# Optimization experiments

Hardware: AMD Instinct MI355X
Metric: run time of the kernel (lower is better)

Reference implementation:

```python
import jax, jax.numpy as jnp
import numpy as np

DIM = 256
HEADS = 8
DIM_HEAD = 32
INNER = HEADS * DIM_HEAD  # 256
SCALE = DIM_HEAD ** -0.5
NEG = -100.0

MASK0 = jnp.array([[0., 0., 0., NEG],
                   [0., 0., NEG, 0.],
                   [0., NEG, 0., 0.],
                   [NEG, 0., 0., 0.]], dtype=jnp.float32)
MASK1 = jnp.array([[0., NEG, 0., NEG],
                   [NEG, 0., NEG, 0.],
                   [NEG, NEG, NEG, NEG],
                   [NEG, NEG, NEG, NEG]], dtype=jnp.float32)


def setup_inputs() -> dict:
    key = jax.random.key(0)
    ks = jax.random.split(key, 8)
    b, p, d = 8, 3136, DIM
    return {
        "x": jax.random.normal(ks[0], (b, p, d), jnp.float32),
        "y": jax.random.normal(ks[1], (b, p, d), jnp.float32),
        "Wqkv_z": jax.random.normal(ks[2], (3 * INNER, d), jnp.float32) * 0.02,
        "Wout_z": jax.random.normal(ks[3], (d, INNER), jnp.float32) * 0.02,
        "bout_z": jnp.zeros((d,), jnp.float32),
        "Wqkv_z1": jax.random.normal(ks[4], (3 * INNER, d), jnp.float32) * 0.02,
        "Wout_z1": jax.random.normal(ks[5], (d, INNER), jnp.float32) * 0.02,
        "bout_z1": jnp.zeros((d,), jnp.float32),
    }


def _attn_stage(z, Wqkv, Wout, bout, mask):
    # z: [b, p, n=4, d]
    b, p, n, d = z.shape
    qkv = jnp.einsum('bpnd,ed->bpne', z, Wqkv)  # [b,p,4,3*inner]
    q, k, v = jnp.split(qkv, 3, axis=-1)
    def heads(t):  # [b,p,n,inner] -> [b,p,h,n,dh]
        return t.reshape(b, p, n, HEADS, DIM_HEAD).transpose(0, 1, 3, 2, 4)
    q, k, v = heads(q), heads(k), heads(v)
    dots = jnp.einsum('bphid,bphjd->bphij', q, k) * SCALE + mask
    attn = jax.nn.softmax(dots, axis=-1)
    out = jnp.einsum('bphij,bphjd->bphid', attn, v)
    out = out.transpose(0, 1, 3, 2, 4).reshape(b, p, n, INNER)
    return jnp.einsum('bpne,de->bpnd', out, Wout) + bout


def reference(x, y, Wqkv_z, Wout_z, bout_z, Wqkv_z1, Wout_z1, bout_z1):
    b, p, d = x.shape
    rgb_g = jnp.mean(x, axis=1, keepdims=True)    # avg_pool1d over p == mean
    dep_g = jnp.mean(y, axis=1, keepdims=True)
    rgb_g = jnp.broadcast_to(rgb_g, (b, p, d))
    dep_g = jnp.broadcast_to(dep_g, (b, p, d))
    z = jnp.stack([x, y, rgb_g, dep_g], axis=2)   # [b,p,4,d]
    z_out = _attn_stage(z, Wqkv_z, Wout_z, bout_z, MASK0)
    z_out1 = _attn_stage(z_out, Wqkv_z1, Wout_z1, bout_z1, MASK1)
    x1 = z_out1[:, :, 0, :]
    y1 = z_out1[:, :, 1, :]
    return (x1, y1)
```

## Files before the change

### kernel.cpp

```cpp
#include <hip/hip_runtime.h>
#include <hip/hip_fp8.h>

typedef unsigned short u16;
typedef unsigned int   u32;
typedef unsigned char  u8;
typedef short bf16x8 __attribute__((ext_vector_type(8)));
typedef float f32x16 __attribute__((ext_vector_type(16)));

#define NB    8
#define NP    3136
#define DIM   256
#define PTILE 16
#define NEGM  (-100.0f)
#define QKSCALE 0.17677669529663687f

#define LDS_SZ  65536
#define Q0B     16384
#define K0B     32768
#define P0B     49152
#define A1LB    32768
#define Q1B     49152
#define P1B     32768
#define AO1LB   16384

__device__ __forceinline__ float bflo(u32 w) { return __uint_as_float(w << 16); }
__device__ __forceinline__ float bfhi(u32 w) { return __uint_as_float(w & 0xffff0000u); }

__device__ __forceinline__ u32 cvt_pk(float a, float b) {
  u32 r;
  asm("v_cvt_pk_bf16_f32 %0, %1, %2" : "=v"(r) : "v"(a), "v"(b));
  return r;
}
__device__ __forceinline__ u8 f2fp8(float v) {
  __hip_fp8_e4m3 t(v);
  return *(u8*)&t;
}
__device__ __forceinline__ float fp82f(u8 bv) {
  __hip_fp8_e4m3 t;
  *(u8*)&t = bv;
  return (float)t;
}
__device__ __forceinline__ bf16x8 expand8(uint2 u) {
  const float s = 0.00390625f;
  float f0 = fp82f((u8)(u.x))       * s, f1 = fp82f((u8)(u.x >> 8))  * s;
  float f2 = fp82f((u8)(u.x >> 16)) * s, f3 = fp82f((u8)(u.x >> 24)) * s;
  float f4 = fp82f((u8)(u.y))       * s, f5 = fp82f((u8)(u.y >> 8))  * s;
  float f6 = fp82f((u8)(u.y >> 16)) * s, f7 = fp82f((u8)(u.y >> 24)) * s;
  union { bf16x8 v; uint4 w; } r;
  r.w.x = cvt_pk(f0, f1); r.w.y = cvt_pk(f2, f3);
  r.w.z = cvt_pk(f4, f5); r.w.w = cvt_pk(f6, f7);
  return r.v;
}

__device__ __forceinline__ void phase_fence() { __builtin_amdgcn_sched_barrier(0); }

template<int MASKI>
__device__ __forceinline__ float maskv(int i, int j) {
  if (MASKI == 0) return ((i ^ j) == 3) ? NEGM : 0.f;
  return (i >= 2 || ((i ^ j) & 1)) ? NEGM : 0.f;
}

#define FRAG(nt, ks) ((((size_t)(nt) * 16 + (ks)) * 64 + lane) * 8)

__device__ __forceinline__ void pack4(const float* __restrict__ W,
                                      u16* __restrict__ hi, u16* __restrict__ lo,
                                      int is_qkv, int pair0, int tid) {
  const int p    = pair0 + (tid >> 6);
  const int lane = tid & 63;
  const int nt = p >> 4, ks = p & 15;
  const int n  = nt * 32 + (lane & 31);
  const int k0 = ks * 16 + ((lane >> 5) << 3);
  const float scale = (is_qkv && n < 256) ? QKSCALE : 1.0f;
  const float* src = W + (size_t)n * 256 + k0;
  const size_t o = (((size_t)nt * 16 + ks) * 64 + lane) * 8;
#pragma unroll
  for (int j = 0; j < 8; j++) {
    float v = src[j] * scale;
    u32 wh = cvt_pk(v, v);
    hi[o + j] = (u16)wh;
    if (lo) lo[o + j] = (u16)cvt_pk(v - bflo(wh), 0.f);
  }
}

__global__ __launch_bounds__(256)
void prep1(const float* __restrict__ x, const float* __restrict__ y,
           float* __restrict__ part,
           const float* __restrict__ wqkv0, u16* __restrict__ wq0_hi,
           const float* __restrict__ wout1, u16* __restrict__ wo1_hi, u16* __restrict__ wo1_lo,
           const float* __restrict__ wqkv1, const float* __restrict__ wout0,
           float* __restrict__ Wc,
           const float* __restrict__ bout0, float* __restrict__ bq) {
  __shared__ float srow[256];
  const int bid = blockIdx.x;
  const int tid = threadIdx.x;
  if (bid < 512) {
    const int chunk = bid & 31;
    const int ab = bid >> 5;
    const int b = ab & 7;
    const float* src = (ab >> 3) ? y : x;
    float s = 0.f;
    const int p0 = chunk * 98;
    for (int i = 0; i < 98; i++)
      s += src[((size_t)b * NP + p0 + i) * DIM + tid];
    part[((size_t)ab * 32 + chunk) * DIM + tid] = s;
  } else if (bid < 608) {
    pack4(wqkv0, wq0_hi, nullptr, 1, (bid - 512) * 4, tid);
  } else if (bid < 640) {
    pack4(wout1, wo1_hi, wo1_lo, 0, (bid - 608) * 4, tid);
  } else if (bid < 1408) {
    const int n = bid - 640;
    srow[tid] = wqkv1[(size_t)n * 256 + tid];
    __syncthreads();
    float acc = 0.f;
#pragma unroll 8
    for (int d = 0; d < 256; d++)
      acc += srow[d] * wout0[(size_t)d * 256 + tid];
    Wc[(size_t)n * 256 + tid] = acc;
  } else {
    const int n = (bid - 1408) * 256 + tid;
    float s = 0.f;
    for (int d = 0; d < 256; d += 4) {
      const float4 w = *(const float4*)(wqkv1 + (size_t)n * 256 + d);
      const float4 bv = *(const float4*)(bout0 + d);
      s += w.x * bv.x + w.y * bv.y + w.z * bv.z + w.w * bv.w;
    }
    bq[n] = (n < 256) ? s * QKSCALE : s;
  }
}

__global__ __launch_bounds__(256)
void prep2(const float* __restrict__ part, float* __restrict__ g,
           const float* __restrict__ Wc, u16* __restrict__ wc_hi, u16* __restrict__ wc_lo) {
  const int bid = blockIdx.x;
  const int tid = threadIdx.x;
  if (bid < 16) {
    float s = 0.f;
    for (int c = 0; c < 32; c++) s += part[((size_t)bid * 32 + c) * DIM + tid];
    g[bid * DIM + tid] = s * (1.0f / 3136.0f);
  } else {
    pack4(Wc, wc_hi, wc_lo, 1, (bid - 16) * 4, tid);
  }
}

__global__ __launch_bounds__(256)
void prep3(const float* __restrict__ g, const float* __restrict__ wqkv0,
           float* __restrict__ qkvg) {
  __shared__ float srow[256];
  const int bt = blockIdx.x;
  const int b = bt >> 1, t = bt & 1;
  const int tid = threadIdx.x;
  srow[tid] = g[(t == 0 ? b : 8 + b) * 256 + tid];
  __syncthreads();
#pragma unroll
  for (int s = 0; s < 3; s++) {
    const int e = s * 256 + tid;
    float acc = 0.f;
    for (int d = 0; d < 256; d += 4) {
      const float4 w = *(const float4*)(wqkv0 + (size_t)e * 256 + d);
      acc += w.x * srow[d] + w.y * srow[d + 1] + w.z * srow[d + 2] + w.w * srow[d + 3];
    }
    qkvg[(size_t)bt * 768 + e] = (e < 256) ? acc * QKSCALE : acc;
  }
}

__global__ __launch_bounds__(512, 4)
void fused_kernel(const float* __restrict__ x, const float* __restrict__ y,
                  const float* __restrict__ qkvg, float* __restrict__ outp,
                  const u16* __restrict__ wq0_hi,
                  const u16* __restrict__ wc_hi,  const u16* __restrict__ wc_lo,
                  const u16* __restrict__ wo1_hi, const u16* __restrict__ wo1_lo,
                  const float* __restrict__ bq,   const float* __restrict__ bout1) {
  extern __shared__ char lds[];
  const int tid  = threadIdx.x;
  const int lane = tid & 63;
  const int wave = tid >> 6;
  const int cl   = lane & 31;
  const int rh5  = lane >> 5;
  const int kgrp = rh5 << 3;
  const int b    = blockIdx.y;
  const int pos0 = blockIdx.x * PTILE;
  const int apos = wave * 2 + rh5;
  const int ah   = (lane >> 2) & 7;
  const int adq  = lane & 3;
  const float* qg = qkvg + (size_t)(b * 2) * 768;

  {
    const int r   = tid >> 4;
    const int cb  = (tid & 15) * 16;
    const int pos = pos0 + (r >> 1);
    const float* src = ((r & 1) ? y : x) + ((size_t)b * NP + pos) * DIM;
#pragma unroll
    for (int u = 0; u < 4; u++) {
      const int col = cb + u * 4;
      float4 v = *(const float4*)(src + col);
      uint2 hw;
      hw.x = cvt_pk(v.x, v.y);
      hw.y = cvt_pk(v.z, v.w);
      *(uint2*)(lds + ((r * 512 + col * 2) ^ ((r & 15) << 4))) = hw;
    }
  }
  __syncthreads();
  phase_fence();

  f32x16 av;
  {
    f32x16 aq, ak;
#pragma unroll
    for (int i = 0; i < 16; i++) { aq[i] = 0.f; ak[i] = 0.f; av[i] = 0.f; }
#pragma unroll 2
    for (int ks = 0; ks < 16; ks++) {
      const int k0 = ks * 16 + kgrp;
      bf16x8 ahf = *(const bf16x8*)(lds + ((cl * 512 + k0 * 2) ^ ((cl & 15) << 4)));
      bf16x8 bQ = *(const bf16x8*)(wq0_hi + FRAG(wave, ks));
      bf16x8 bK = *(const bf16x8*)(wq0_hi + FRAG(8 + wave, ks));
      bf16x8 bV = *(const bf16x8*)(wq0_hi + FRAG(16 + wave, ks));
      __builtin_amdgcn_s_setprio(1);
      aq = __builtin_amdgcn_mfma_f32_32x32x16_bf16(ahf, bQ, aq, 0, 0, 0);
      ak = __builtin_amdgcn_mfma_f32_32x32x16_bf16(ahf, bK, ak, 0, 0, 0);
      av = __builtin_amdgcn_mfma_f32_32x32x16_bf16(ahf, bV, av, 0, 0, 0);
      __builtin_amdgcn_s_setprio(0);
    }
    const int sw0 = ((cl ^ wave) & 7) << 3;
    const int bQd = Q0B + wave * 2048 + cl * 64;
    const int bKd = K0B + wave * 2048 + cl * 64;
#pragma unroll
    for (int gq = 0; gq < 4; gq++) {
      const int p20 = 8 * gq + 4 * rh5;
      uint2 wv;
      wv.x = cvt_pk(aq[4 * gq + 0], aq[4 * gq + 1]);
      wv.y = cvt_pk(aq[4 * gq + 2], aq[4 * gq + 3]);
      *(uint2*)(lds + bQd + ((p20 * 2) ^ sw0)) = wv;
      wv.x = cvt_pk(ak[4 * gq + 0], ak[4 * gq + 1]);
      wv.y = cvt_pk(ak[4 * gq + 2], ak[4 * gq + 3]);
      *(uint2*)(lds + bKd + ((p20 * 2) ^ sw0)) = wv;
    }
  }
  __syncthreads();
  phase_fence();

  {
    const int e0 = ah * 32 + adq * 8;
    float dots[4][4];
#pragma unroll
    for (int i = 0; i < 4; i++)
#pragma unroll
      for (int j = 0; j < 4; j++) dots[i][j] = 0.f;
#pragma unroll 2
    for (int dd = 0; dd < 8; dd++) {
      const int d = adq * 8 + dd;
      const int sw = ((d ^ ah) & 7) << 3;
      u32 qw = *(const u32*)(lds + Q0B + ah * 2048 + d * 64 + ((apos * 4) ^ sw));
      u32 kw = *(const u32*)(lds + K0B + ah * 2048 + d * 64 + ((apos * 4) ^ sw));
      float q[4] = { bflo(qw), bfhi(qw), qg[e0 + dd], qg[768 + e0 + dd] };
      float k[4] = { bflo(kw), bfhi(kw), qg[256 + e0 + dd], qg[1024 + e0 + dd] };
#pragma unroll
      for (int i = 0; i < 4; i++)
#pragma unroll
        for (int j = 0; j < 4; j++) dots[i][j] += q[i] * k[j];
    }
#pragma unroll
    for (int i = 0; i < 4; i++)
#pragma unroll
      for (int j = 0; j < 4; j++) {
        float s = dots[i][j];
        s += __shfl_xor(s, 1);
        s += __shfl_xor(s, 2);
        dots[i][j] = s + maskv<0>(i, j);
      }
    if (adq == 0) {
#pragma unroll
      for (int i = 0; i < 4; i++) {
        const float mx = fmaxf(fmaxf(dots[i][0], dots[i][1]), fmaxf(dots[i][2], dots[i][3]));
        const float e0_ = __expf(dots[i][0] - mx), e1_ = __expf(dots[i][1] - mx);
        const float e2_ = __expf(dots[i][2] - mx), e3_ = __expf(dots[i][3] - mx);
        const float inv = 1.f / (e0_ + e1_ + e2_ + e3_);
        float4 pv_ = { e0_ * inv, e1_ * inv, e2_ * inv, e3_ * inv };
        *(float4*)(lds + P0B + ((apos * 8 + ah) * 4 + i) * 16) = pv_;
      }
    }
  }
  __syncthreads();
  phase_fence();

  {
    const float vg2 = qg[512 + wave * 32 + cl];
    const float vg3 = qg[768 + 512 + wave * 32 + cl];
    const int c = wave * 32 + cl;
#pragma unroll
    for (int gq = 0; gq < 4; gq++) {
#pragma unroll
      for (int pp = 0; pp < 2; pp++) {
        const int pos = 4 * gq + 2 * rh5 + pp;
        const float v0 = av[4 * gq + 2 * pp], v1 = av[4 * gq + 2 * pp + 1];
#pragma unroll
        for (int i = 0; i < 4; i++) {
          float4 pi = *(const float4*)(lds + P0B + ((pos * 8 + wave) * 4 + i) * 16);
          const float o = pi.x * v0 + pi.y * v1 + pi.z * vg2 + pi.w * vg3;
          const int R = pos * 4 + i;
          const u32 hw_ = cvt_pk(o, o);
          *(u16*)(lds + ((R * 512 + c * 2) ^ ((R & 15) << 4))) = (u16)hw_;
          *(u8*)(lds + A1LB + ((R * 256 + c) ^ ((R & 15) << 3))) =
              f2fp8((o - bflo(hw_)) * 256.f);
        }
      }
    }
  }
  __syncthreads();
  phase_fence();

  {
    f32x16 aq0, aq1;
#pragma unroll
    for (int i = 0; i < 16; i++) { aq0[i] = 0.f; aq1[i] = 0.f; }
#pragma unroll 1
    for (int ks = 0; ks < 16; ks++) {
      const int k0 = ks * 16 + kgrp;
      bf16x8 ah0 = *(const bf16x8*)(lds + ((cl * 512 + k0 * 2) ^ ((cl & 15) << 4)));
      bf16x8 ah1 = *(const bf16x8*)(lds + (((32 + cl) * 512 + k0 * 2) ^ (((32 + cl) & 15) << 4)));
      bf16x8 bh = *(const bf16x8*)(wc_hi + FRAG(wave, ks));
      bf16x8 bl = *(const bf16x8*)(wc_lo + FRAG(wave, ks));
      __builtin_amdgcn_s_setprio(1);
      aq0 = __builtin_amdgcn_mfma_f32_32x32x16_bf16(ah0, bh, aq0, 0, 0, 0);
      aq0 = __builtin_amdgcn_mfma_f32_32x32x16_bf16(ah0, bl, aq0, 0, 0, 0);
      aq1 = __builtin_amdgcn_mfma_f32_32x32x16_bf16(ah1, bh, aq1, 0, 0, 0);
      aq1 = __builtin_amdgcn_mfma_f32_32x32x16_bf16(ah1, bl, aq1, 0, 0, 0);
      __builtin_amdgcn_s_setprio(0);
    }
    const float qb = bq[wave * 32 + cl];
    const int swq = ((cl ^ wave) & 7) << 3;
    const int bQ1 = Q1B + wave * 2048 + cl * 64;
#pragma unroll
    for (int gq = 0; gq < 4; gq++) {
      const int posA = 2 * gq + rh5;
      *(u32*)(lds + bQ1 + ((posA * 4) ^ swq)) =
          cvt_pk(aq0[4 * gq] + qb, aq0[4 * gq + 1] + qb);
      *(u32*)(lds + bQ1 + (((posA + 8) * 4) ^ swq)) =
          cvt_pk(aq1[4 * gq] + qb, aq1[4 * gq + 1] + qb);
    }
  }
  phase_fence();
  uint2 kp0[4], kp1[4];
  {
    f32x16 ak0, ak1;
#pragma unroll
    for (int i = 0; i < 16; i++) { ak0[i] = 0.f; ak1[i] = 0.f; }
#pragma unroll 1
    for (int ks = 0; ks < 16; ks++) {
      const int k0 = ks * 16 + kgrp;
      bf16x8 ah0 = *(const bf16x8*)(lds + ((cl * 512 + k0 * 2) ^ ((cl & 15) << 4)));
      bf16x8 ah1 = *(const bf16x8*)(lds + (((32 + cl) * 512 + k0 * 2) ^ (((32 + cl) & 15) << 4)));
      bf16x8 bh = *(const bf16x8*)(wc_hi + FRAG(8 + wave, ks));
      bf16x8 bl = *(const bf16x8*)(wc_lo + FRAG(8 + wave, ks));
      __builtin_amdgcn_s_setprio(1);
      ak0 = __builtin_amdgcn_mfma_f32_32x32x16_bf16(ah0, bh, ak0, 0, 0, 0);
      ak0 = __builtin_amdgcn_mfma_f32_32x32x16_bf16(ah0, bl, ak0, 0, 0, 0);
      ak1 = __builtin_amdgcn_mfma_f32_32x32x16_bf16(ah1, bh, ak1, 0, 0, 0);
      ak1 = __builtin_amdgcn_mfma_f32_32x32x16_bf16(ah1, bl, ak1, 0, 0, 0);
      __builtin_amdgcn_s_setprio(0);
    }
    const float kb = bq[256 + wave * 32 + cl];
#pragma unroll
    for (int gq = 0; gq < 4; gq++) {
      kp0[gq].x = cvt_pk(ak0[4 * gq + 0] + kb, ak0[4 * gq + 1] + kb);
      kp0[gq].y = cvt_pk(ak0[4 * gq + 2] + kb, ak0[4 * gq + 3] + kb);
      kp1[gq].x = cvt_pk(ak1[4 * gq + 0] + kb, ak1[4 * gq + 1] + kb);
      kp1[gq].y = cvt_pk(ak1[4 * gq + 2] + kb, ak1[4 * gq + 3] + kb);
    }
  }
  phase_fence();
  f32x16 av0, av1;
  {
#pragma unroll
    for (int i = 0; i < 16; i++) { av0[i] = 0.f; av1[i] = 0.f; }
#pragma unroll 1
    for (int ks = 0; ks < 16; ks++) {
      const int k0 = ks * 16 + kgrp;
      bf16x8 ah0 = *(const bf16x8*)(lds + ((cl * 512 + k0 * 2) ^ ((cl & 15) << 4)));
      bf16x8 ah1 = *(const bf16x8*)(lds + (((32 + cl) * 512 + k0 * 2) ^ (((32 + cl) & 15) << 4)));
      uint2 u0 = *(const uint2*)(lds + A1LB + ((cl * 256 + k0) ^ ((cl & 15) << 3)));
      uint2 u1 = *(const uint2*)(lds + A1LB + (((32 + cl) * 256 + k0) ^ (((32 + cl) & 15) << 3)));
      bf16x8 al0 = expand8(u0);
      bf16x8 al1 = expand8(u1);
      bf16x8 bh = *(const bf16x8*)(wc_hi + FRAG(16 + wave, ks));
      bf16x8 bl = *(const bf16x8*)(wc_lo + FRAG(16 + wave, ks));
      __builtin_amdgcn_s_setprio(1);
      av0 = __builtin_amdgcn_mfma_f32_32x32x16_bf16(ah0, bh, av0, 0, 0, 0);
      av0 = __builtin_amdgcn_mfma_f32_32x32x16_bf16(ah0, bl, av0, 0, 0, 0);
      av0 = __builtin_amdgcn_mfma_f32_32x32x16_bf16(al0, bh, av0, 0, 0, 0);
      av1 = __builtin_amdgcn_mfma_f32_32x32x16_bf16(ah1, bh, av1, 0, 0, 0);
      av1 = __builtin_amdgcn_mfma_f32_32x32x16_bf16(ah1, bl, av1, 0, 0, 0);
      av1 = __builtin_amdgcn_mfma_f32_32x32x16_bf16(al1, bh, av1, 0, 0, 0);
      __builtin_amdgcn_s_setprio(0);
    }
    const float vb = bq[512 + wave * 32 + cl];
#pragma unroll
    for (int i = 0; i < 16; i++) { av0[i] += vb; av1[i] += vb; }
  }
  __syncthreads();
  phase_fence();

  {
    const int swk = ((cl ^ wave) & 7) << 4;
    const int bK1 = wave * 4096 + cl * 128;
#pragma unroll
    for (int gq = 0; gq < 4; gq++) {
      const int R0a = 8 * gq + 4 * rh5;
      *(uint2*)(lds + bK1 + ((R0a * 2) ^ swk)) = kp0[gq];
      *(uint2*)(lds + bK1 + (((R0a + 32) * 2) ^ swk)) = kp1[gq];
    }
  }
  __syncthreads();
  phase_fence();

  {
    float dots[2][4];
#pragma unroll
    for (int i = 0; i < 2; i++)
#pragma unroll
      for (int j = 0; j < 4; j++) dots[i][j] = 0.f;
#pragma unroll 2
    for (int dd = 0; dd < 8; dd++) {
      const int d = adq * 8 + dd;
      u32 qw = *(const u32*)(lds + Q1B + ah * 2048 + d * 64 +
                             ((apos * 4) ^ (((d ^ ah) & 7) << 3)));
      uint2 kw = *(const uint2*)(lds + ah * 4096 + d * 128 +
                                 ((apos * 8) ^ (((d ^ ah) & 7) << 4)));
      float q[2] = { bflo(qw), bfhi(qw) };
      float k[4] = { bflo(kw.x), bfhi(kw.x), bflo(kw.y), bfhi(kw.y) };
#pragma unroll
      for (int i = 0; i < 2; i++)
#pragma unroll
        for (int j = 0; j < 4; j++) dots[i][j] += q[i] * k[j];
    }
#pragma unroll
    for (int i = 0; i < 2; i++)
#pragma unroll
      for (int j = 0; j < 4; j++) {
        float s = dots[i][j];
        s += __shfl_xor(s, 1);
        s += __shfl_xor(s, 2);
        dots[i][j] = s + maskv<1>(i, j);
      }
    if (adq == 0) {
#pragma unroll
      for (int i = 0; i < 2; i++) {
        const float mx = fmaxf(fmaxf(dots[i][0], dots[i][1]), fmaxf(dots[i][2], dots[i][3]));
        const float e0_ = __expf(dots[i][0] - mx), e1_ = __expf(dots[i][1] - mx);
        const float e2_ = __expf(dots[i][2] - mx), e3_ = __expf(dots[i][3] - mx);
        const float inv = 1.f / (e0_ + e1_ + e2_ + e3_);
        float4 pv_ = { e0_ * inv, e1_ * inv, e2_ * inv, e3_ * inv };
        *(float4*)(lds + P1B + ((apos * 8 + ah) * 2 + i) * 16) = pv_;
      }
    }
  }
  __syncthreads();
  phase_fence();

  {
    const int c = wave * 32 + cl;
#pragma unroll
    for (int gq = 0; gq < 4; gq++) {
      const int posA = 2 * gq + rh5;
#pragma unroll
      for (int i = 0; i < 2; i++) {
        float4 pa = *(const float4*)(lds + P1B + ((posA * 8 + wave) * 2 + i) * 16);
        const float o0 = pa.x * av0[4 * gq] + pa.y * av0[4 * gq + 1] +
                         pa.z * av0[4 * gq + 2] + pa.w * av0[4 * gq + 3];
        const int r0 = posA * 2 + i;
        const u32 h0 = cvt_pk(o0, o0);
        const int bo0 = (r0 * 512 + c * 2) ^ ((r0 & 15) << 4);
        *(u16*)(lds + bo0) = (u16)h0;
        *(u16*)(lds + AO1LB + bo0) = (u16)cvt_pk(o0 - bflo(h0), 0.f);
        float4 pb = *(const float4*)(lds + P1B + (((posA + 8) * 8 + wave) * 2 + i) * 16);
        const float o1 = pb.x * av1[4 * gq] + pb.y * av1[4 * gq + 1] +
                         pb.z * av1[4 * gq + 2] + pb.w * av1[4 * gq + 3];
        const int r1 = (posA + 8) * 2 + i;
        const u32 h1 = cvt_pk(o1, o1);
        const int bo1 = (r1 * 512 + c * 2) ^ ((r1 & 15) << 4);
        *(u16*)(lds + bo1) = (u16)h1;
        *(u16*)(lds + AO1LB + bo1) = (u16)cvt_pk(o1 - bflo(h1), 0.f);
      }
    }
  }
  __syncthreads();
  phase_fence();

  {
    f32x16 acc2;
#pragma unroll
    for (int i = 0; i < 16; i++) acc2[i] = 0.f;
#pragma unroll 2
    for (int ks = 0; ks < 16; ks++) {
      const int k0 = ks * 16 + kgrp;
      const int bo = (cl * 512 + k0 * 2) ^ ((cl & 15) << 4);
      bf16x8 ahf = *(const bf16x8*)(lds + bo);
      bf16x8 alf = *(const bf16x8*)(lds + AO1LB + bo);
      bf16x8 bh = *(const bf16x8*)(wo1_hi + FRAG(wave, ks));
      bf16x8 bl = *(const bf16x8*)(wo1_lo + FRAG(wave, ks));
      __builtin_amdgcn_s_setprio(1);
      acc2 = __builtin_amdgcn_mfma_f32_32x32x16_bf16(ahf, bh, acc2, 0, 0, 0);
      acc2 = __builtin_amdgcn_mfma_f32_32x32x16_bf16(ahf, bl, acc2, 0, 0, 0);
      acc2 = __builtin_amdgcn_mfma_f32_32x32x16_bf16(alf, bh, acc2, 0, 0, 0);
      __builtin_amdgcn_s_setprio(0);
    }
    const int c = wave * 32 + cl;
    const float bc = bout1[c];
    const size_t TOT = (size_t)NB * NP * DIM;
#pragma unroll
    for (int i = 0; i < 16; i++) {
      const int r = (i & 3) + ((i >> 2) << 3) + 4 * rh5;
      const int pos = pos0 + (r >> 1);
      const float v = acc2[i] + bc;
      if ((r & 1) == 0) outp[((size_t)b * NP + pos) * DIM + c] = v;
      else              outp[TOT + ((size_t)b * NP + pos) * DIM + c] = v;
    }
  }
}

extern "C" void kernel_launch(void* const* d_in, const int* in_sizes, int n_in,
                              void* d_out, int out_size, void* d_ws, size_t ws_size,
                              hipStream_t stream) {
  const float* x     = (const float*)d_in[0];
  const float* y     = (const float*)d_in[1];
  const float* wqkv0 = (const float*)d_in[2];
  const float* wout0 = (const float*)d_in[3];
  const float* bout0 = (const float*)d_in[4];
  const float* wqkv1 = (const float*)d_in[5];
  const float* wout1 = (const float*)d_in[6];
  const float* bout1 = (const float*)d_in[7];

  float* part = (float*)d_ws;
  float* g    = part + (size_t)16 * 32 * DIM;
  float* Wc   = g + 16 * DIM;
  float* bq   = Wc + (size_t)768 * 256;
  float* qkvg = bq + 768;
  u16* w = (u16*)(qkvg + (size_t)8 * 2 * 768);
  u16* wq0_hi = w; w += (size_t)768 * 256;
  u16* wc_hi  = w; w += (size_t)768 * 256;
  u16* wc_lo  = w; w += (size_t)768 * 256;
  u16* wo1_hi = w; w += (size_t)256 * 256;
  u16* wo1_lo = w; w += (size_t)256 * 256;

  prep1<<<dim3(1411), dim3(256), 0, stream>>>(
      x, y, part, wqkv0, wq0_hi, wout1, wo1_hi, wo1_lo,
      wqkv1, wout0, Wc, bout0, bq);
  prep2<<<dim3(112), dim3(256), 0, stream>>>(part, g, Wc, wc_hi, wc_lo);
  prep3<<<dim3(16), dim3(256), 0, stream>>>(g, wqkv0, qkvg);

  fused_kernel<<<dim3(NP / PTILE, NB), dim3(512), LDS_SZ, stream>>>(
      x, y, qkvg, (float*)d_out,
      wq0_hi, wc_hi, wc_lo, wo1_hi, wo1_lo, bq, bout1);
}
```

Baseline: 238.9 us.

## Drop fp8 low-part correction, merge prep3 into prep2, finer mean partials

Removes the fp8-encoded low residual of the stage-1 attention output and its extra MFMA per k-step, so the activation is kept only in bf16 with a hi/lo split on the weights. Merges the global-mean finalisation and the global QKV projection into one kernel, which removes a launch. Splits the mean reduction into more, smaller chunks so prep1 has more parallelism. The first change cuts MFMA work, LDS traffic and conversion ALU in the hot kernel at the cost of lower precision in the second-stage QKV projection.

New measurement: 221.8 us. 7.1% less time.

```diff
diff --git a/kernel.cpp b/kernel.cpp
--- a/kernel.cpp
+++ b/kernel.cpp
@@ -1,9 +1,7 @@
 #include <hip/hip_runtime.h>
-#include <hip/hip_fp8.h>
 
 typedef unsigned short u16;
 typedef unsigned int   u32;
-typedef unsigned char  u8;
 typedef short bf16x8 __attribute__((ext_vector_type(8)));
 typedef float f32x16 __attribute__((ext_vector_type(16)));
 
@@ -18,7 +16,6 @@
 #define Q0B     16384
 #define K0B     32768
 #define P0B     49152
-#define A1LB    32768
 #define Q1B     49152
 #define P1B     32768
 #define AO1LB   16384
@@ -30,26 +27,6 @@
   u32 r;
   asm("v_cvt_pk_bf16_f32 %0, %1, %2" : "=v"(r) : "v"(a), "v"(b));
   return r;
-}
-__device__ __forceinline__ u8 f2fp8(float v) {
-  __hip_fp8_e4m3 t(v);
-  return *(u8*)&t;
-}
-__device__ __forceinline__ float fp82f(u8 bv) {
-  __hip_fp8_e4m3 t;
-  *(u8*)&t = bv;
-  return (float)t;
-}
-__device__ __forceinline__ bf16x8 expand8(uint2 u) {
-  const float s = 0.00390625f;
-  float f0 = fp82f((u8)(u.x))       * s, f1 = fp82f((u8)(u.x >> 8))  * s;
-  float f2 = fp82f((u8)(u.x >> 16)) * s, f3 = fp82f((u8)(u.x >> 24)) * s;
-  float f4 = fp82f((u8)(u.y))       * s, f5 = fp82f((u8)(u.y >> 8))  * s;
-  float f6 = fp82f((u8)(u.y >> 16)) * s, f7 = fp82f((u8)(u.y >> 24)) * s;
-  union { bf16x8 v; uint4 w; } r;
-  r.w.x = cvt_pk(f0, f1); r.w.y = cvt_pk(f2, f3);
-  r.w.z = cvt_pk(f4, f5); r.w.w = cvt_pk(f6, f7);
-  return r.v;
 }
 
 __device__ __forceinline__ void phase_fence() { __builtin_amdgcn_sched_barrier(0); }
@@ -93,22 +70,23 @@
   __shared__ float srow[256];
   const int bid = blockIdx.x;
   const int tid = threadIdx.x;
-  if (bid < 512) {
-    const int chunk = bid & 31;
-    const int ab = bid >> 5;
+  if (bid < 1568) {
+    const int ab = bid / 98;
+    const int chunk = bid - ab * 98;
     const int b = ab & 7;
     const float* src = (ab >> 3) ? y : x;
     float s = 0.f;
-    const int p0 = chunk * 98;
-    for (int i = 0; i < 98; i++)
+    const int p0 = chunk * 32;
+#pragma unroll 4
+    for (int i = 0; i < 32; i++)
       s += src[((size_t)b * NP + p0 + i) * DIM + tid];
-    part[((size_t)ab * 32 + chunk) * DIM + tid] = s;
-  } else if (bid < 608) {
-    pack4(wqkv0, wq0_hi, nullptr, 1, (bid - 512) * 4, tid);
-  } else if (bid < 640) {
-    pack4(wout1, wo1_hi, wo1_lo, 0, (bid - 608) * 4, tid);
-  } else if (bid < 1408) {
-    const int n = bid - 640;
+    part[((size_t)ab * 98 + chunk) * DIM + tid] = s;
+  } else if (bid < 1664) {
+    pack4(wqkv0, wq0_hi, nullptr, 1, (bid - 1568) * 4, tid);
+  } else if (bid < 1696) {
+    pack4(wout1, wo1_hi, wo1_lo, 0, (bid - 1664) * 4, tid);
+  } else if (bid < 2464) {
+    const int n = bid - 1696;
     srow[tid] = wqkv1[(size_t)n * 256 + tid];
     __syncthreads();
     float acc = 0.f;
@@ -117,7 +95,7 @@
       acc += srow[d] * wout0[(size_t)d * 256 + tid];
     Wc[(size_t)n * 256 + tid] = acc;
   } else {
-    const int n = (bid - 1408) * 256 + tid;
+    const int n = (bid - 2464) * 256 + tid;
     float s = 0.f;
     for (int d = 0; d < 256; d += 4) {
       const float4 w = *(const float4*)(wqkv1 + (size_t)n * 256 + d);
@@ -129,37 +107,30 @@
 }
 
 __global__ __launch_bounds__(256)
-void prep2(const float* __restrict__ part, float* __restrict__ g,
+void prep2(const float* __restrict__ part, const float* __restrict__ wqkv0,
+           float* __restrict__ qkvg,
            const float* __restrict__ Wc, u16* __restrict__ wc_hi, u16* __restrict__ wc_lo) {
+  __shared__ float srow[256];
   const int bid = blockIdx.x;
   const int tid = threadIdx.x;
   if (bid < 16) {
     float s = 0.f;
-    for (int c = 0; c < 32; c++) s += part[((size_t)bid * 32 + c) * DIM + tid];
-    g[bid * DIM + tid] = s * (1.0f / 3136.0f);
+    for (int c = 0; c < 98; c++) s += part[((size_t)bid * 98 + c) * DIM + tid];
+    srow[tid] = s * (1.0f / 3136.0f);
+    __syncthreads();
+    const int bt = (bid < 8) ? (2 * bid) : (2 * (bid - 8) + 1);
+#pragma unroll
+    for (int sct = 0; sct < 3; sct++) {
+      const int e = sct * 256 + tid;
+      float acc = 0.f;
+      for (int d = 0; d < 256; d += 4) {
+        const float4 w = *(const float4*)(wqkv0 + (size_t)e * 256 + d);
+        acc += w.x * srow[d] + w.y * srow[d + 1] + w.z * srow[d + 2] + w.w * srow[d + 3];
+      }
+      qkvg[(size_t)bt * 768 + e] = (e < 256) ? acc * QKSCALE : acc;
+    }
   } else {
     pack4(Wc, wc_hi, wc_lo, 1, (bid - 16) * 4, tid);
-  }
-}
-
-__global__ __launch_bounds__(256)
-void prep3(const float* __restrict__ g, const float* __restrict__ wqkv0,
-           float* __restrict__ qkvg) {
-  __shared__ float srow[256];
-  const int bt = blockIdx.x;
-  const int b = bt >> 1, t = bt & 1;
-  const int tid = threadIdx.x;
-  srow[tid] = g[(t == 0 ? b : 8 + b) * 256 + tid];
-  __syncthreads();
-#pragma unroll
-  for (int s = 0; s < 3; s++) {
-    const int e = s * 256 + tid;
-    float acc = 0.f;
-    for (int d = 0; d < 256; d += 4) {
-      const float4 w = *(const float4*)(wqkv0 + (size_t)e * 256 + d);
-      acc += w.x * srow[d] + w.y * srow[d + 1] + w.z * srow[d + 2] + w.w * srow[d + 3];
-    }
-    qkvg[(size_t)bt * 768 + e] = (e < 256) ? acc * QKSCALE : acc;
   }
 }
 
@@ -297,10 +268,7 @@
           float4 pi = *(const float4*)(lds + P0B + ((pos * 8 + wave) * 4 + i) * 16);
           const float o = pi.x * v0 + pi.y * v1 + pi.z * vg2 + pi.w * vg3;
           const int R = pos * 4 + i;
-          const u32 hw_ = cvt_pk(o, o);
-          *(u16*)(lds + ((R * 512 + c * 2) ^ ((R & 15) << 4))) = (u16)hw_;
-          *(u8*)(lds + A1LB + ((R * 256 + c) ^ ((R & 15) << 3))) =
-              f2fp8((o - bflo(hw_)) * 256.f);
+          *(u16*)(lds + ((R * 512 + c * 2) ^ ((R & 15) << 4))) = (u16)cvt_pk(o, o);
         }
       }
     }
@@ -377,19 +345,13 @@
       const int k0 = ks * 16 + kgrp;
       bf16x8 ah0 = *(const bf16x8*)(lds + ((cl * 512 + k0 * 2) ^ ((cl & 15) << 4)));
       bf16x8 ah1 = *(const bf16x8*)(lds + (((32 + cl) * 512 + k0 * 2) ^ (((32 + cl) & 15) << 4)));
-      uint2 u0 = *(const uint2*)(lds + A1LB + ((cl * 256 + k0) ^ ((cl & 15) << 3)));
-      uint2 u1 = *(const uint2*)(lds + A1LB + (((32 + cl) * 256 + k0) ^ (((32 + cl) & 15) << 3)));
-      bf16x8 al0 = expand8(u0);
-      bf16x8 al1 = expand8(u1);
       bf16x8 bh = *(const bf16x8*)(wc_hi + FRAG(16 + wave, ks));
       bf16x8 bl = *(const bf16x8*)(wc_lo + FRAG(16 + wave, ks));
       __builtin_amdgcn_s_setprio(1);
       av0 = __builtin_amdgcn_mfma_f32_32x32x16_bf16(ah0, bh, av0, 0, 0, 0);
       av0 = __builtin_amdgcn_mfma_f32_32x32x16_bf16(ah0, bl, av0, 0, 0, 0);
-      av0 = __builtin_amdgcn_mfma_f32_32x32x16_bf16(al0, bh, av0, 0, 0, 0);
       av1 = __builtin_amdgcn_mfma_f32_32x32x16_bf16(ah1, bh, av1, 0, 0, 0);
       av1 = __builtin_amdgcn_mfma_f32_32x32x16_bf16(ah1, bl, av1, 0, 0, 0);
-      av1 = __builtin_amdgcn_mfma_f32_32x32x16_bf16(al1, bh, av1, 0, 0, 0);
       __builtin_amdgcn_s_setprio(0);
     }
     const float vb = bq[512 + wave * 32 + cl];
@@ -530,8 +492,7 @@
   const float* bout1 = (const float*)d_in[7];
 
   float* part = (float*)d_ws;
-  float* g    = part + (size_t)16 * 32 * DIM;
-  float* Wc   = g + 16 * DIM;
+  float* Wc   = part + (size_t)16 * 98 * DIM;
   float* bq   = Wc + (size_t)768 * 256;
   float* qkvg = bq + 768;
   u16* w = (u16*)(qkvg + (size_t)8 * 2 * 768);
@@ -541,11 +502,10 @@
   u16* wo1_hi = w; w += (size_t)256 * 256;
   u16* wo1_lo = w; w += (size_t)256 * 256;
 
-  prep1<<<dim3(1411), dim3(256), 0, stream>>>(
+  prep1<<<dim3(2467), dim3(256), 0, stream>>>(
       x, y, part, wqkv0, wq0_hi, wout1, wo1_hi, wo1_lo,
       wqkv1, wout0, Wc, bout0, bq);
-  prep2<<<dim3(112), dim3(256), 0, stream>>>(part, g, Wc, wc_hi, wc_lo);
-  prep3<<<dim3(16), dim3(256), 0, stream>>>(g, wqkv0, qkvg);
+  prep2<<<dim3(112), dim3(256), 0, stream>>>(part, wqkv0, qkvg, Wc, wc_hi, wc_lo);
 
   fused_kernel<<<dim3(NP / PTILE, NB), dim3(512), LDS_SZ, stream>>>(
       x, y, qkvg, (float*)d_out,
```
